# Kernel optimization log

Hardware: AMD Instinct MI355X
Metric: run time of the kernel (lower is better)

## Reference

```python
import jax, jax.numpy as jnp
import numpy as np
import math

EPS = 1e-6
TEMPERATURE = 1.0
NEG = -100.0


def setup_inputs() -> dict:
    key = jax.random.key(0)
    k1, k2, k3 = jax.random.split(key, 3)
    B, N, C = 16, 2048, 64
    x = jax.random.normal(k1, (B, N, C), dtype=jnp.float32)
    y = jax.random.normal(k2, (B, N, C), dtype=jnp.float32)
    # complementary keep / pruned gates, as produced by the TPS token scorer
    keep = jax.random.bernoulli(k3, 0.5, (B, N, 1)).astype(jnp.float32)
    pruned = 1.0 - keep
    return {
        "x": x,
        "y": y,
        "current_keep_decision": keep,
        "current_pruned_decision": pruned,
    }


def reference(x, y, current_keep_decision, current_pruned_decision):
    # Training branch of TPSModule.forward (module defaults to training mode).
    B, N, C = x.shape
    # --- get_sim(x, None, mask_eye=-100, l2_norm=True) ---
    xn = x / (jnp.linalg.norm(x, axis=-1, keepdims=True) + EPS)
    sim = jnp.einsum("bnc,bmc->bnm", xn, xn)  # [B, N, N]
    eye = jnp.eye(N, dtype=bool)
    sim = jnp.where(eye[None, :, :], NEG, sim)
    sim = sim / TEMPERATURE
    # mask out columns of non-kept tokens
    keep_b = current_keep_decision.reshape(B, 1, N).astype(bool)
    sim = jnp.where(keep_b, sim, NEG)
    # hard top-1 (with ties) per row, gated by pruned flag of the source row
    sim_th = jnp.max(sim, axis=2, keepdims=True)  # [B, N, 1]
    mask = (sim == sim_th).astype(x.dtype) * current_pruned_decision  # [B, N, N]
    cos = mask * sim
    # transpose: now rows index destination (kept) tokens
    mask_t = mask.transpose(0, 2, 1)
    cos_t = cos.transpose(0, 2, 1)
    numerator = jnp.exp(cos_t) * mask_t  # [B, N, N]
    denominator = math.e + jnp.sum(numerator, axis=-1, keepdims=True)  # [B, N, 1]
    out = x * (math.e / denominator) + jnp.einsum(
        "bnm,bmc->bnc", numerator / denominator, x
    )
    return out
```

## Files before the change

kernel.cpp:

```cpp
#include <hip/hip_runtime.h>
#include <math.h>

#define BB 16
#define NN 2048
#define CC 64
#define TPB 256
#define MROWS 32
#define RPW 8
#define E_CONST 2.71828182845904523536f

__global__ __launch_bounds__(TPB) void k_pre(const float* __restrict__ keep,
                                             float* __restrict__ outz,
                                             float* __restrict__ S,
                                             int* __restrict__ cntP,
                                             int* __restrict__ cntK,
                                             int* __restrict__ listP,
                                             int* __restrict__ listK) {
    const int tid = threadIdx.x, lane = tid & 63;

    float4* o4 = (float4*)outz + (size_t)blockIdx.x * 1024;
    float4 z = {0.0f, 0.0f, 0.0f, 0.0f};
#pragma unroll
    for (int i = 0; i < 4; ++i) o4[i * TPB + tid] = z;

    const int b = blockIdx.x;
    if (b >= BB) return;

    __shared__ int cP, cK;
    if (tid == 0) { cP = 0; cK = 0; }
    __syncthreads();
    for (int i = tid; i < NN; i += TPB) S[b * NN + i] = 0.0f;
    const unsigned long long lt = (lane == 63) ? 0x7fffffffffffffffull
                                               : ((1ull << lane) - 1ull);
#pragma unroll
    for (int it = 0; it < NN / TPB; ++it) {
        int n = it * TPB + tid;
        bool kp = keep[b * NN + n] != 0.0f;
        unsigned long long mk = __ballot(kp);
        int nk = __popcll(mk);
        int bk = 0, bp = 0;
        if (lane == 0) {
            bk = atomicAdd(&cK, nk);
            bp = atomicAdd(&cP, 64 - nk);
        }
        bk = __shfl(bk, 0); bp = __shfl(bp, 0);
        int pk = __popcll(mk & lt);
        if (kp) listK[b * NN + bk + pk] = n;
        else    listP[b * NN + bp + (lane - pk)] = n;
    }
    __syncthreads();
    if (tid == 0) { cntP[b] = cP; cntK[b] = cK; }
}

__global__ __launch_bounds__(TPB) void k_pre2(const float* __restrict__ x,
                                              const int* __restrict__ cntK,
                                              const int* __restrict__ listK,
                                              float* __restrict__ colMf) {
    const int b    = blockIdx.x & 15;
    const int seg  = blockIdx.x >> 4;
    const int lane = threadIdx.x & 63;
    const int wid  = threadIdx.x >> 6;
    const int wave = seg * 4 + wid;
    const int K    = cntK[b];
    const int Kend = min(NN, K + 128);

    const float* xb = x + (size_t)b * NN * CC;
    float* cf = colMf + (size_t)b * 16 * NN * 4;

    for (int colp = wave; colp < Kend; colp += 256) {
        float v = 0.0f;
        if (colp < K) {
            int tok = listK[b * NN + colp];
            float xv = xb[(size_t)tok * CC + lane];
            float sq = xv * xv;
#pragma unroll
            for (int off = 32; off; off >>= 1) sq += __shfl_xor(sq, off, 64);
            v = xv / (sqrtf(sq) + 1e-6f);
        }
        cf[((size_t)(lane >> 2) * NN + colp) * 4 + (lane & 3)] = v;
    }
}

template <int J>
__device__ __forceinline__ void tile_body(const float4* __restrict__ x4,
                                          const float4* __restrict__ cm,
                                          const int* rtok, int cstart, int K,
                                          int lane, float* tmax,
                                          unsigned long long* msk) {
    float acc[RPW][J];
#pragma unroll
    for (int r = 0; r < RPW; ++r)
#pragma unroll
        for (int j = 0; j < J; ++j) acc[r][j] = 0.0f;

#pragma unroll 2
    for (int k4 = 0; k4 < 16; ++k4) {
        float4 rv[RPW];
#pragma unroll
        for (int r = 0; r < RPW; ++r)
            rv[r] = x4[(size_t)rtok[r] * 16 + k4];
        const float4* cmk = cm + (size_t)k4 * NN + cstart + lane;
        float4 cv[J];
#pragma unroll
        for (int j = 0; j < J; ++j)
            cv[j] = cmk[j * 64];
#pragma unroll
        for (int r = 0; r < RPW; ++r)
#pragma unroll
            for (int j = 0; j < J; ++j)
                acc[r][j] = fmaf(rv[r].x, cv[j].x,
                            fmaf(rv[r].y, cv[j].y,
                            fmaf(rv[r].z, cv[j].z,
                            fmaf(rv[r].w, cv[j].w, acc[r][j]))));
    }

    const int cb0 = cstart >> 6;
#pragma unroll
    for (int r = 0; r < RPW; ++r)
#pragma unroll
        for (int j = 0; j < J; ++j) {
            int colp = cstart + j * 64 + lane;
            float s = (colp < K) ? acc[r][j] : -1.0e30f;
            unsigned long long bit = 1ull << (cb0 + j);
            if (s > tmax[r])       { tmax[r] = s; msk[r] = bit; }
            else if (s == tmax[r])  msk[r] |= bit;
        }
}

__global__ __launch_bounds__(TPB) void k_argmax(
    const float* __restrict__ x,
    const float4* __restrict__ colM,
    const int*   __restrict__ cntP,
    const int*   __restrict__ cntK,
    const int*   __restrict__ listP,
    const int*   __restrict__ listK,
    float* __restrict__ S,
    float* __restrict__ A) {

    const int b    = blockIdx.x & 15;
    const int tile = blockIdx.x >> 4;
    const int P = cntP[b], K = cntK[b];
    const int base = tile * MROWS;
    if (base >= P) return;

    const int tid = threadIdx.x;
    const int wid = tid >> 6;
    const int lane = tid & 63;

    int rtok[RPW];
#pragma unroll
    for (int r = 0; r < RPW; ++r) {
        int rid = base + wid * RPW + r;
        int tok = (rid < P) ? listP[b * NN + rid] : 0;
        rtok[r] = __builtin_amdgcn_readfirstlane(tok);
    }
    const float4* x4 = (const float4*)(x + (size_t)b * NN * CC);
    const float4* cm = colM + (size_t)b * 16 * NN;

    float              tmax[RPW];
    unsigned long long msk[RPW];
#pragma unroll
    for (int r = 0; r < RPW; ++r) { tmax[r] = -3.0e38f; msk[r] = 0ull; }

    int cstart = 0;
    while (cstart < K) {
        int rem = K - cstart;
        if (rem > 128) {
            tile_body<4>(x4, cm, rtok, cstart, K, lane, tmax, msk);
            cstart += 256;
        } else {
            tile_body<2>(x4, cm, rtok, cstart, K, lane, tmax, msk);
            cstart += 128;
        }
    }

    int nvr = P - base - wid * RPW;
    for (int r = 0; r < RPW; ++r) {
        if (r >= nvr) break;
        float m = tmax[r];
#pragma unroll
        for (int off = 32; off; off >>= 1) m = fmaxf(m, __shfl_xor(m, off, 64));
        int src = rtok[r];
        float xv = x[(size_t)(b * NN + src) * CC + lane];
        float sq = xv * xv;
#pragma unroll
        for (int off = 32; off; off >>= 1) sq += __shfl_xor(sq, off, 64);
        float ivr = 1.0f / (sqrtf(sq) + 1e-6f);
        float wgt = expf(m * ivr);
        unsigned long long bal = __ballot(tmax[r] == m && msk[r] != 0ull);
        while (bal) {
            int sl = __ffsll(bal) - 1;
            bal &= bal - 1;
            unsigned long long mm = __shfl(msk[r], sl);
            while (mm) {
                int cb = __ffsll(mm) - 1;
                mm &= mm - 1;
                int colp = (cb << 6) + sl;
                int dst = listK[b * NN + colp];
                atomicAdd(&A[(size_t)(b * NN + dst) * CC + lane], wgt * xv);
                if (lane == 0) atomicAdd(&S[b * NN + dst], wgt);
            }
        }
    }
}

__global__ __launch_bounds__(TPB) void k_finalize(const float* __restrict__ x,
                                                  const float* __restrict__ S,
                                                  float* __restrict__ out) {
    int i = blockIdx.x * TPB + threadIdx.x;
    int row = i >> 4;
    float inv = 1.0f / (E_CONST + S[row]);
    float4 xv = ((const float4*)x)[i];
    float4 av = ((float4*)out)[i];
    float4 o;
    o.x = (xv.x * E_CONST + av.x) * inv;
    o.y = (xv.y * E_CONST + av.y) * inv;
    o.z = (xv.z * E_CONST + av.z) * inv;
    o.w = (xv.w * E_CONST + av.w) * inv;
    ((float4*)out)[i] = o;
}

extern "C" void kernel_launch(void* const* d_in, const int* in_sizes, int n_in,
                              void* d_out, int out_size, void* d_ws, size_t ws_size,
                              hipStream_t stream) {
    const float* x    = (const float*)d_in[0];
    const float* keep = (const float*)d_in[2];
    float* out = (float*)d_out;

    char* ws = (char*)d_ws;
    float* S    = (float*)(ws + (128 << 10));
    int*   cntP = (int*)(ws + (256 << 10));
    int*   cntK = cntP + 16;
    int*   listP = (int*)(ws + (256 << 10) + 128);
    int*   listK = listP + BB * NN;
    float* colMf = (float*)(ws + (1 << 20));

    k_pre<<<512, TPB, 0, stream>>>(keep, out, S, cntP, cntK, listP, listK);

    k_pre2<<<BB * 64, TPB, 0, stream>>>(x, cntK, listK, colMf);

    k_argmax<<<(NN / MROWS) * BB, TPB, 0, stream>>>(x, (const float4*)colMf,
                                                    cntP, cntK, listP, listK,
                                                    S, out);

    k_finalize<<<(BB * NN * CC / 4) / TPB, TPB, 0, stream>>>(x, S, out);
}
```

Baseline: 149.2 us.

## Stage column tiles in LDS with double-buffered async global-to-LDS loads

The argmax kernel now copies each chunk of normalized kept-token columns into shared memory once per block, using global_load_lds, instead of having each of the four waves read the same columns from global memory. Loads for the next 4-k4 chunk overlap with compute on the current one through a two-slot buffer, with block barriers between chunks. The aim is to remove redundant cache traffic and hide load latency. The cost is 32 KB of LDS per block, which may reduce occupancy, plus a barrier per chunk, and correctness depends on the barriers waiting for the async LDS writes to finish.

```diff
diff --git a/kernel.cpp b/kernel.cpp
--- a/kernel.cpp
+++ b/kernel.cpp
@@ -81,29 +81,38 @@
     }
 }
 
+__device__ __forceinline__ void gll16(const void* g, void* l) {
+    __builtin_amdgcn_global_load_lds(
+        (const __attribute__((address_space(1))) void*)g,
+        (__attribute__((address_space(3))) void*)l, 16, 0, 0);
+}
+
+__device__ __forceinline__ void stage_chunk(const float4* __restrict__ cm,
+                                            int cstart, int kbase, int W4,
+                                            float4 (*buf)[256],
+                                            int wid, int lane) {
+    const float4* g = cm + (size_t)(kbase + wid) * NN + cstart + lane;
+#pragma unroll
+    for (int j = 0; j < 4; ++j)
+        if (j < W4) gll16(g + j * 64, &buf[wid][j * 64]);
+}
+
 template <int J>
-__device__ __forceinline__ void tile_body(const float4* __restrict__ x4,
-                                          const float4* __restrict__ cm,
-                                          const int* rtok, int cstart, int K,
-                                          int lane, float* tmax,
-                                          unsigned long long* msk) {
-    float acc[RPW][J];
-#pragma unroll
-    for (int r = 0; r < RPW; ++r)
-#pragma unroll
-        for (int j = 0; j < J; ++j) acc[r][j] = 0.0f;
-
-#pragma unroll 2
-    for (int k4 = 0; k4 < 16; ++k4) {
+__device__ __forceinline__ void compute_chunk(const float4* __restrict__ x4,
+                                              const int* rtok,
+                                              const float4 (*buf)[256],
+                                              int kbase, float acc[RPW][J],
+                                              int lane) {
+#pragma unroll
+    for (int k4l = 0; k4l < 4; ++k4l) {
         float4 rv[RPW];
 #pragma unroll
         for (int r = 0; r < RPW; ++r)
-            rv[r] = x4[(size_t)rtok[r] * 16 + k4];
-        const float4* cmk = cm + (size_t)k4 * NN + cstart + lane;
+            rv[r] = x4[(size_t)rtok[r] * 16 + kbase + k4l];
         float4 cv[J];
 #pragma unroll
         for (int j = 0; j < J; ++j)
-            cv[j] = cmk[j * 64];
+            cv[j] = buf[k4l][j * 64 + lane];
 #pragma unroll
         for (int r = 0; r < RPW; ++r)
 #pragma unroll
@@ -112,6 +121,30 @@
                             fmaf(rv[r].y, cv[j].y,
                             fmaf(rv[r].z, cv[j].z,
                             fmaf(rv[r].w, cv[j].w, acc[r][j]))));
+    }
+}
+
+template <int J>
+__device__ __forceinline__ void do_tile(const float4* __restrict__ x4,
+                                        const float4* __restrict__ cm,
+                                        const int* rtok, int cstart, int K,
+                                        int lane, int wid,
+                                        float4 (*sbuf)[4][256],
+                                        float* tmax, unsigned long long* msk) {
+    float acc[RPW][J];
+#pragma unroll
+    for (int r = 0; r < RPW; ++r)
+#pragma unroll
+        for (int j = 0; j < J; ++j) acc[r][j] = 0.0f;
+
+    stage_chunk(cm, cstart, 0, J, sbuf[0], wid, lane);
+    __syncthreads();
+#pragma unroll
+    for (int c = 0; c < 4; ++c) {
+        if (c < 3)
+            stage_chunk(cm, cstart, (c + 1) * 4, J, sbuf[(c + 1) & 1], wid, lane);
+        compute_chunk<J>(x4, rtok, sbuf[c & 1], c * 4, acc, lane);
+        __syncthreads();
     }
 
     const int cb0 = cstart >> 6;
@@ -143,6 +176,8 @@
     const int base = tile * MROWS;
     if (base >= P) return;
 
+    __shared__ float4 sbuf[2][4][256];
+
     const int tid = threadIdx.x;
     const int wid = tid >> 6;
     const int lane = tid & 63;
@@ -166,10 +201,10 @@
     while (cstart < K) {
         int rem = K - cstart;
         if (rem > 128) {
-            tile_body<4>(x4, cm, rtok, cstart, K, lane, tmax, msk);
+            do_tile<4>(x4, cm, rtok, cstart, K, lane, wid, sbuf, tmax, msk);
             cstart += 256;
         } else {
-            tile_body<2>(x4, cm, rtok, cstart, K, lane, tmax, msk);
+            do_tile<2>(x4, cm, rtok, cstart, K, lane, wid, sbuf, tmax, msk);
             cstart += 128;
         }
     }
```

Result: slower. 309.9 us (+107.8%).

## Split argmax columns across waves with 8-row blocks and shared-memory max

Applied to the files above, without the earlier changes.

The argmax kernel now gives each block 8 pruned rows instead of 32. Its four waves split the kept columns into interleaved 128-column tiles, rather than each wave taking its own 8 rows over all columns. Per-wave row maxima are combined through shared memory with one block barrier, and each wave then scatters only the tied columns it owns. This launches about four times as many active blocks and shortens each wave's serial column loop, which should improve latency hiding and balance. The cost is an extra barrier and shared-memory reduction per block, and only the 2-wide tile body is used now.

```diff
diff --git a/kernel.cpp b/kernel.cpp
--- a/kernel.cpp
+++ b/kernel.cpp
@@ -5,8 +5,7 @@
 #define NN 2048
 #define CC 64
 #define TPB 256
-#define MROWS 32
-#define RPW 8
+#define MROWS 8
 #define E_CONST 2.71828182845904523536f
 
 __global__ __launch_bounds__(TPB) void k_pre(const float* __restrict__ keep,
@@ -87,17 +86,17 @@
                                           const int* rtok, int cstart, int K,
                                           int lane, float* tmax,
                                           unsigned long long* msk) {
-    float acc[RPW][J];
-#pragma unroll
-    for (int r = 0; r < RPW; ++r)
+    float acc[MROWS][J];
+#pragma unroll
+    for (int r = 0; r < MROWS; ++r)
 #pragma unroll
         for (int j = 0; j < J; ++j) acc[r][j] = 0.0f;
 
 #pragma unroll 2
     for (int k4 = 0; k4 < 16; ++k4) {
-        float4 rv[RPW];
-#pragma unroll
-        for (int r = 0; r < RPW; ++r)
+        float4 rv[MROWS];
+#pragma unroll
+        for (int r = 0; r < MROWS; ++r)
             rv[r] = x4[(size_t)rtok[r] * 16 + k4];
         const float4* cmk = cm + (size_t)k4 * NN + cstart + lane;
         float4 cv[J];
@@ -105,7 +104,7 @@
         for (int j = 0; j < J; ++j)
             cv[j] = cmk[j * 64];
 #pragma unroll
-        for (int r = 0; r < RPW; ++r)
+        for (int r = 0; r < MROWS; ++r)
 #pragma unroll
             for (int j = 0; j < J; ++j)
                 acc[r][j] = fmaf(rv[r].x, cv[j].x,
@@ -116,7 +115,7 @@
 
     const int cb0 = cstart >> 6;
 #pragma unroll
-    for (int r = 0; r < RPW; ++r)
+    for (int r = 0; r < MROWS; ++r)
 #pragma unroll
         for (int j = 0; j < J; ++j) {
             int colp = cstart + j * 64 + lane;
@@ -147,47 +146,47 @@
     const int wid = tid >> 6;
     const int lane = tid & 63;
 
-    int rtok[RPW];
-#pragma unroll
-    for (int r = 0; r < RPW; ++r) {
-        int rid = base + wid * RPW + r;
+    int rtok[MROWS];
+#pragma unroll
+    for (int r = 0; r < MROWS; ++r) {
+        int rid = base + r;
         int tok = (rid < P) ? listP[b * NN + rid] : 0;
         rtok[r] = __builtin_amdgcn_readfirstlane(tok);
     }
     const float4* x4 = (const float4*)(x + (size_t)b * NN * CC);
     const float4* cm = colM + (size_t)b * 16 * NN;
 
-    float              tmax[RPW];
-    unsigned long long msk[RPW];
-#pragma unroll
-    for (int r = 0; r < RPW; ++r) { tmax[r] = -3.0e38f; msk[r] = 0ull; }
-
-    int cstart = 0;
-    while (cstart < K) {
-        int rem = K - cstart;
-        if (rem > 128) {
-            tile_body<4>(x4, cm, rtok, cstart, K, lane, tmax, msk);
-            cstart += 256;
-        } else {
-            tile_body<2>(x4, cm, rtok, cstart, K, lane, tmax, msk);
-            cstart += 128;
-        }
-    }
-
-    int nvr = P - base - wid * RPW;
-    for (int r = 0; r < RPW; ++r) {
-        if (r >= nvr) break;
+    float              tmax[MROWS];
+    unsigned long long msk[MROWS];
+#pragma unroll
+    for (int r = 0; r < MROWS; ++r) { tmax[r] = -3.0e38f; msk[r] = 0ull; }
+
+    const int NT = (K + 127) >> 7;
+    for (int t = wid; t < NT; t += 4)
+        tile_body<2>(x4, cm, rtok, t << 7, K, lane, tmax, msk);
+
+    __shared__ float mW[MROWS][4];
+    const int nvr = min(MROWS, P - base);
+#pragma unroll
+    for (int r = 0; r < MROWS; ++r) {
         float m = tmax[r];
 #pragma unroll
         for (int off = 32; off; off >>= 1) m = fmaxf(m, __shfl_xor(m, off, 64));
+        if (lane == 0) mW[r][wid] = m;
+    }
+    __syncthreads();
+
+    for (int r = 0; r < nvr; ++r) {
+        float M = fmaxf(fmaxf(mW[r][0], mW[r][1]), fmaxf(mW[r][2], mW[r][3]));
+        unsigned long long bal = __ballot(tmax[r] == M && msk[r] != 0ull);
+        if (bal == 0ull) continue;
         int src = rtok[r];
         float xv = x[(size_t)(b * NN + src) * CC + lane];
         float sq = xv * xv;
 #pragma unroll
         for (int off = 32; off; off >>= 1) sq += __shfl_xor(sq, off, 64);
         float ivr = 1.0f / (sqrtf(sq) + 1e-6f);
-        float wgt = expf(m * ivr);
-        unsigned long long bal = __ballot(tmax[r] == m && msk[r] != 0ull);
+        float wgt = expf(M * ivr);
         while (bal) {
             int sl = __ffsll(bal) - 1;
             bal &= bal - 1;
```

New measurement: 140.8 us. 1.06x faster.
